# Optimization experiments

Measured on AMD Instinct MI355X. Metric: run time of the kernel, lower is better.

The kernel has to match this reference:

```python
import jax, jax.numpy as jnp
import numpy as np

D_MODEL = 1024
N_HEADS = 16
D_K = D_MODEL // N_HEADS


def setup_inputs() -> dict:
    key = jax.random.key(0)
    ks = jax.random.split(key, 9)
    s = 0.02
    x = jax.random.normal(ks[0], (2, 2048, D_MODEL), dtype=jnp.float32)
    Wq = jax.random.normal(ks[1], (D_MODEL, D_MODEL), dtype=jnp.float32) * s
    bq = jax.random.normal(ks[2], (D_MODEL,), dtype=jnp.float32) * s
    Wk = jax.random.normal(ks[3], (D_MODEL, D_MODEL), dtype=jnp.float32) * s
    bk = jax.random.normal(ks[4], (D_MODEL,), dtype=jnp.float32) * s
    Wv = jax.random.normal(ks[5], (D_MODEL, D_MODEL), dtype=jnp.float32) * s
    bv = jax.random.normal(ks[6], (D_MODEL,), dtype=jnp.float32) * s
    Wo = jax.random.normal(ks[7], (D_MODEL, D_MODEL), dtype=jnp.float32) * s
    bo = jax.random.normal(ks[8], (D_MODEL,), dtype=jnp.float32) * s
    return {"x": x, "Wq": Wq, "bq": bq, "Wk": Wk, "bk": bk,
            "Wv": Wv, "bv": bv, "Wo": Wo, "bo": bo}


def reference(x, Wq, bq, Wk, bk, Wv, bv, Wo, bo):
    B, S, D = x.shape
    # nn.Linear: y = x @ W.T + b
    q = x @ Wq.T + bq  # [B,S,D]
    k = x @ Wk.T + bk
    v = x @ Wv.T + bv
    # split heads -> [B,H,S,dk]
    q = q.reshape(B, S, N_HEADS, D_K).transpose(0, 2, 1, 3)
    k = k.reshape(B, S, N_HEADS, D_K).transpose(0, 2, 1, 3)
    v = v.reshape(B, S, N_HEADS, D_K).transpose(0, 2, 1, 3)
    scale = 1.0 / jnp.sqrt(jnp.asarray(D_K, dtype=x.dtype))
    scores = jnp.einsum('bhqd,bhkd->bhqk', q, k) * scale  # [B,H,S,S]
    weights = jax.nn.softmax(scores, axis=-1)
    out = jnp.einsum('bhqk,bhkd->bhqd', weights, v)  # [B,H,S,dk]
    concat = out.transpose(0, 2, 1, 3).reshape(B, S, D)
    return concat @ Wo.T + bo
```

## Files before the change

kernel.cpp:

```cpp
#include <hip/hip_runtime.h>

typedef unsigned short ushort_t;
typedef __attribute__((ext_vector_type(8))) __bf16 bf16x8;
typedef __attribute__((ext_vector_type(4))) short short4v;
typedef __attribute__((ext_vector_type(4))) float floatx4;

#define AS1 __attribute__((address_space(1)))
#define AS3 __attribute__((address_space(3)))

#define D_MODEL 1024
#define NH 16
#define DKH 64
#define SEQ 2048
#define NB 2
#define MTOT (NB * SEQ)

#define QSCALE 0.18033688011112042f

#define OFF_X   0u
#define OFF_WQ  4194304u
#define OFF_BQ  5242880u
#define OFF_WK  5243904u
#define OFF_BK  6292480u
#define OFF_WV  6293504u
#define OFF_BV  7342080u
#define OFF_WO  7343104u
#define OFF_BO  8391680u
#define CVT_TOT 8392704u

#define MFMA16(a, b, c) __builtin_amdgcn_mfma_f32_16x16x16bf16_1k((a), (b), (c), 0, 0, 0)

__device__ __forceinline__ float bf2f(ushort_t u) {
    union { unsigned u; float f; } v; v.u = ((unsigned)u) << 16; return v.f;
}
__device__ __forceinline__ ushort_t f2bf(float f) {
    union { float f; unsigned u; } v; v.f = f;
    unsigned r = v.u + 0x7FFFu + ((v.u >> 16) & 1u);
    return (ushort_t)(r >> 16);
}
__device__ __forceinline__ unsigned pack2bf(float a, float b) {
    unsigned ua = __float_as_uint(a), ub = __float_as_uint(b);
    ua = ua + 0x7FFFu + ((ua >> 16) & 1u);
    ub = ub + 0x7FFFu + ((ub >> 16) & 1u);
    return __builtin_amdgcn_perm(ub, ua, 0x07060302);
}
__device__ __forceinline__ short4v pack4bf(floatx4 v) {
    union { uint2 u; short4v s; } cv;
    cv.u.x = pack2bf(v[0], v[1]);
    cv.u.y = pack2bf(v[2], v[3]);
    return cv.s;
}

__global__ __launch_bounds__(256) void convert_kernel(
    const float* __restrict__ x,  const float* __restrict__ wq, const float* __restrict__ bq_,
    const float* __restrict__ wk, const float* __restrict__ bk_, const float* __restrict__ wv,
    const float* __restrict__ bv_, const float* __restrict__ wo, const float* __restrict__ bo_,
    ushort_t* __restrict__ dst)
{
    const unsigned idx = ((unsigned)blockIdx.x * 256u + threadIdx.x) * 4u;
    if (idx >= CVT_TOT) return;
    const float* src; unsigned off;
    if      (idx < OFF_WQ) { src = x;   off = idx - OFF_X;  }
    else if (idx < OFF_BQ) { src = wq;  off = idx - OFF_WQ; }
    else if (idx < OFF_WK) { src = bq_; off = idx - OFF_BQ; }
    else if (idx < OFF_BK) { src = wk;  off = idx - OFF_WK; }
    else if (idx < OFF_WV) { src = bk_; off = idx - OFF_BK; }
    else if (idx < OFF_BV) { src = wv;  off = idx - OFF_WV; }
    else if (idx < OFF_WO) { src = bv_; off = idx - OFF_BV; }
    else if (idx < OFF_BO) { src = wo;  off = idx - OFF_WO; }
    else                   { src = bo_; off = idx - OFF_BO; }
    float4 v = *reinterpret_cast<const float4*>(src + off);
    uint2 p;
    p.x = pack2bf(v.x, v.y);
    p.y = pack2bf(v.z, v.w);
    *reinterpret_cast<uint2*>(dst + idx) = p;
}

__device__ __forceinline__ void gemm_core(
    const ushort_t* __restrict__ X, const ushort_t* __restrict__ W,
    int m0, int n0, ushort_t* lds, floatx4 acc[4][4])
{
    const int tid = threadIdx.x;
    const int lane = tid & 63, wv = tid >> 6;
    const int wm = (wv >> 1) * 64, wn = (wv & 1) * 64;
    const int l15 = lane & 15, quad = lane >> 4;
    const floatx4 z4 = {0.f, 0.f, 0.f, 0.f};
#pragma unroll
    for (int i = 0; i < 4; ++i)
#pragma unroll
        for (int j = 0; j < 4; ++j) acc[i][j] = z4;
    const int lrow = lane >> 2;
    const int lcol = (lane & 3) * 8;
    const ushort_t* gA = X + (size_t)(m0 + lrow) * D_MODEL + lcol;
    const ushort_t* gB = W + (size_t)(n0 + lrow) * D_MODEL + lcol;
    for (int k0 = 0; k0 < D_MODEL; k0 += 64) {
        __syncthreads();
#pragma unroll
        for (int j = 0; j < 2; ++j) {
            const int r0 = (wv * 2 + j) * 16;
            __builtin_amdgcn_global_load_lds(
                (const AS1 unsigned*)(gA + (size_t)r0 * D_MODEL + k0),
                (AS3 unsigned*)(lds + r0 * 32), 16, 0, 0);
            __builtin_amdgcn_global_load_lds(
                (const AS1 unsigned*)(gA + (size_t)r0 * D_MODEL + k0 + 32),
                (AS3 unsigned*)(lds + 4096 + r0 * 32), 16, 0, 0);
            __builtin_amdgcn_global_load_lds(
                (const AS1 unsigned*)(gB + (size_t)r0 * D_MODEL + k0),
                (AS3 unsigned*)(lds + 8192 + r0 * 32), 16, 0, 0);
            __builtin_amdgcn_global_load_lds(
                (const AS1 unsigned*)(gB + (size_t)r0 * D_MODEL + k0 + 32),
                (AS3 unsigned*)(lds + 12288 + r0 * 32), 16, 0, 0);
        }
        asm volatile("s_waitcnt vmcnt(0)" ::: "memory");
        __syncthreads();
#pragma unroll
        for (int ks = 0; ks < 2; ++ks) {
            const ushort_t* A = lds + ks * 4096;
            const ushort_t* B = lds + 8192 + ks * 4096;
            bf16x8 af[4], bfr[4];
#pragma unroll
            for (int i = 0; i < 4; ++i)
                af[i] = *reinterpret_cast<const bf16x8*>(A + (wm + i * 16 + l15) * 32 + quad * 8);
#pragma unroll
            for (int j = 0; j < 4; ++j)
                bfr[j] = *reinterpret_cast<const bf16x8*>(B + (wn + j * 16 + l15) * 32 + quad * 8);
#pragma unroll
            for (int i = 0; i < 4; ++i)
#pragma unroll
                for (int j = 0; j < 4; ++j)
                    acc[i][j] = __builtin_amdgcn_mfma_f32_16x16x32_bf16(af[i], bfr[j], acc[i][j], 0, 0, 0);
        }
    }
}

__global__ __launch_bounds__(256, 3) void qkv_kernel(
    const ushort_t* __restrict__ x,
    const ushort_t* __restrict__ Wq, const ushort_t* __restrict__ bq,
    const ushort_t* __restrict__ Wk, const ushort_t* __restrict__ bk,
    const ushort_t* __restrict__ Wv, const ushort_t* __restrict__ bv,
    ushort_t* __restrict__ q_ws, ushort_t* __restrict__ k_ws, ushort_t* __restrict__ vt_ws)
{
    __shared__ __align__(16) ushort_t lds[17408];
    const int m0 = blockIdx.x * 128;
    const int which = blockIdx.y >> 3;
    const int n0 = (blockIdx.y & 7) * 128;
    const ushort_t* W    = (which == 0) ? Wq : (which == 1) ? Wk : Wv;
    const ushort_t* bias = (which == 0) ? bq : (which == 1) ? bk : bv;
    floatx4 acc[4][4];
    gemm_core(x, W, m0, n0, lds, acc);
    const int tid = threadIdx.x, lane = tid & 63, wv = tid >> 6;
    const int wm = (wv >> 1) * 64, wn = (wv & 1) * 64;
    const int l15 = lane & 15, quad = lane >> 4;
    const int b0 = m0 >> 11;
    const int s0 = m0 & (SEQ - 1);
    __syncthreads();
    if (which < 2) {
        ushort_t* Ts = lds;
        ushort_t* dst = (which == 0) ? q_ws : k_ws;
        const float scl = (which == 0) ? QSCALE : 1.0f;
#pragma unroll
        for (int j = 0; j < 4; ++j) {
            int coln = wn + j * 16 + l15;
            float bb = bf2f(bias[n0 + coln]);
#pragma unroll
            for (int i = 0; i < 4; ++i)
#pragma unroll
                for (int r = 0; r < 4; ++r) {
                    int rowm = wm + i * 16 + quad * 4 + r;
                    Ts[rowm * 136 + coln] = f2bf((acc[i][j][r] + bb) * scl);
                }
        }
        __syncthreads();
#pragma unroll
        for (int i = 0; i < 8; ++i) {
            int c = tid + 256 * i;
            int rowm = c >> 4, chunk = c & 15;
            float4 v = *reinterpret_cast<const float4*>(Ts + rowm * 136 + chunk * 8);
            int s = s0 + rowm;
            int n = n0 + chunk * 8, h = n >> 6, d = n & 63;
            *reinterpret_cast<float4*>(dst + (((size_t)(b0 * NH + h)) * SEQ + s) * DKH + d) = v;
        }
    } else {
        ushort_t* Ts = lds;
#pragma unroll
        for (int j = 0; j < 4; ++j) {
            int coln = wn + j * 16 + l15;
            float bb = bf2f(bias[n0 + coln]);
#pragma unroll
            for (int i = 0; i < 4; ++i)
#pragma unroll
                for (int r = 0; r < 4; ++r) {
                    int rowm = wm + i * 16 + quad * 4 + r;
                    Ts[coln * 136 + rowm] = f2bf(acc[i][j][r] + bb);
                }
        }
        __syncthreads();
#pragma unroll
        for (int i = 0; i < 8; ++i) {
            int c = tid + 256 * i;
            int nr = c >> 4, mc = (c & 15) * 8;
            float4 v = *reinterpret_cast<const float4*>(Ts + nr * 136 + mc);
            int n = n0 + nr, h = n >> 6, d = n & 63;
            *reinterpret_cast<float4*>(vt_ws + (((size_t)(b0 * NH + h)) * DKH + d) * SEQ + s0 + mc) = v;
        }
    }
}

__global__ __launch_bounds__(512, 4) void attn_kernel(
    const ushort_t* __restrict__ q_ws, const ushort_t* __restrict__ k_ws,
    const ushort_t* __restrict__ vt_ws, ushort_t* __restrict__ concat)
{
    __shared__ __align__(16) ushort_t sm[18432];
    const int qb = blockIdx.x, bh = blockIdx.y;
    const int tid = threadIdx.x;
    const int lane = tid & 63, wv = tid >> 6;
    const int half = wv >> 2, wq = wv & 3;
    const int l15 = lane & 15, quad = lane >> 4;
    const int ht = tid & 255;

    const ushort_t* Qg = q_ws + ((size_t)bh * SEQ + qb * 128) * DKH;
    const ushort_t* Kg = k_ws + ((size_t)bh * SEQ + half * (SEQ / 2)) * DKH;
    const ushort_t* Vg = vt_ws + (size_t)bh * DKH * SEQ + half * (SEQ / 2);

    ushort_t* Ks  = sm + half * 4608;
    ushort_t* VTs = sm + 9216 + half * 4608;

    const int r0c = ht >> 3,         c0c = (ht & 7) * 8;
    const int r1c = (ht + 256) >> 3, c1c = ((ht + 256) & 7) * 8;

    bf16x8 aq[2][2];
#pragma unroll
    for (int nt = 0; nt < 2; ++nt)
#pragma unroll
        for (int ks = 0; ks < 2; ++ks)
            aq[nt][ks] = *reinterpret_cast<const bf16x8*>(
                Qg + (size_t)(wq * 32 + nt * 16 + l15) * DKH + ks * 32 + quad * 8);

    const floatx4 z4 = {0.f, 0.f, 0.f, 0.f};
    floatx4 o[2][4];
    floatx4 la4[2] = {z4, z4};
#pragma unroll
    for (int nt = 0; nt < 2; ++nt)
#pragma unroll
        for (int dt = 0; dt < 4; ++dt) o[nt][dt] = z4;

    float4 pk0 = *reinterpret_cast<const float4*>(Kg + (size_t)r0c * DKH + c0c);
    float4 pk1 = *reinterpret_cast<const float4*>(Kg + (size_t)r1c * DKH + c1c);
    float4 pv0 = *reinterpret_cast<const float4*>(Vg + (size_t)r0c * SEQ + c0c);
    float4 pv1 = *reinterpret_cast<const float4*>(Vg + (size_t)r1c * SEQ + c1c);

    for (int t = 0; t < 16; ++t) {
        __syncthreads();
        *reinterpret_cast<float4*>(Ks + r0c * 72 + c0c) = pk0;
        *reinterpret_cast<float4*>(Ks + r1c * 72 + c1c) = pk1;
        *reinterpret_cast<float4*>(VTs + r0c * 72 + c0c) = pv0;
        *reinterpret_cast<float4*>(VTs + r1c * 72 + c1c) = pv1;
        __syncthreads();
        if (t < 15) {
            int toff = (t + 1) * 64;
            pk0 = *reinterpret_cast<const float4*>(Kg + (size_t)(toff + r0c) * DKH + c0c);
            pk1 = *reinterpret_cast<const float4*>(Kg + (size_t)(toff + r1c) * DKH + c1c);
            pv0 = *reinterpret_cast<const float4*>(Vg + (size_t)r0c * SEQ + toff + c0c);
            pv1 = *reinterpret_cast<const float4*>(Vg + (size_t)r1c * SEQ + toff + c1c);
        }

        floatx4 st[2][4];
#pragma unroll
        for (int nt = 0; nt < 2; ++nt)
#pragma unroll
            for (int mt = 0; mt < 4; ++mt) st[nt][mt] = z4;
#pragma unroll
        for (int ks = 0; ks < 2; ++ks)
#pragma unroll
            for (int mt = 0; mt < 4; ++mt) {
                bf16x8 akf = *reinterpret_cast<const bf16x8*>(Ks + (mt * 16 + l15) * 72 + ks * 32 + quad * 8);
                st[0][mt] = __builtin_amdgcn_mfma_f32_16x16x32_bf16(akf, aq[0][ks], st[0][mt], 0, 0, 0);
                st[1][mt] = __builtin_amdgcn_mfma_f32_16x16x32_bf16(akf, aq[1][ks], st[1][mt], 0, 0, 0);
            }

        short4v pb[2][4];
#pragma unroll
        for (int nt = 0; nt < 2; ++nt)
#pragma unroll
            for (int mt = 0; mt < 4; ++mt) {
#pragma unroll
                for (int r = 0; r < 4; ++r) st[nt][mt][r] = exp2f(st[nt][mt][r]);
                la4[nt] += st[nt][mt];
                pb[nt][mt] = pack4bf(st[nt][mt]);
            }

#pragma unroll
        for (int mt = 0; mt < 4; ++mt)
#pragma unroll
            for (int dt = 0; dt < 4; ++dt) {
                short4v av = *reinterpret_cast<const short4v*>(VTs + (dt * 16 + l15) * 72 + mt * 16 + quad * 4);
                o[0][dt] = MFMA16(av, pb[0][mt], o[0][dt]);
                o[1][dt] = MFMA16(av, pb[1][mt], o[1][dt]);
            }
    }
    float lsum[2];
#pragma unroll
    for (int nt = 0; nt < 2; ++nt) {
        float s = la4[nt][0] + la4[nt][1] + la4[nt][2] + la4[nt][3];
        s += __shfl_xor(s, 16, 64);
        s += __shfl_xor(s, 32, 64);
        lsum[nt] = s;
    }
    __syncthreads();
    float* Of = (float*)sm;
    float* lf = Of + 64 * 130;
    if (half == 1) {
#pragma unroll
        for (int nt = 0; nt < 2; ++nt) {
            int q = wq * 32 + nt * 16 + l15;
            if (quad == 0) lf[q] = lsum[nt];
#pragma unroll
            for (int dt = 0; dt < 4; ++dt)
#pragma unroll
                for (int r = 0; r < 4; ++r)
                    Of[(dt * 16 + quad * 4 + r) * 130 + q] = o[nt][dt][r];
        }
    }
    __syncthreads();
    if (half == 0) {
        const int b0 = bh >> 4, h = bh & 15;
#pragma unroll
        for (int nt = 0; nt < 2; ++nt) {
            int q = wq * 32 + nt * 16 + l15;
            float linv = 1.f / (lsum[nt] + lf[q]);
            size_t base = ((size_t)(b0 * SEQ + qb * 128 + q)) * D_MODEL + h * DKH;
#pragma unroll
            for (int dt = 0; dt < 4; ++dt) {
                float f0 = (o[nt][dt][0] + Of[(dt * 16 + quad * 4 + 0) * 130 + q]) * linv;
                float f1 = (o[nt][dt][1] + Of[(dt * 16 + quad * 4 + 1) * 130 + q]) * linv;
                float f2 = (o[nt][dt][2] + Of[(dt * 16 + quad * 4 + 2) * 130 + q]) * linv;
                float f3 = (o[nt][dt][3] + Of[(dt * 16 + quad * 4 + 3) * 130 + q]) * linv;
                uint2 pk;
                pk.x = pack2bf(f0, f1);
                pk.y = pack2bf(f2, f3);
                *reinterpret_cast<uint2*>(concat + base + dt * 16 + quad * 4) = pk;
            }
        }
    }
}

__global__ __launch_bounds__(256, 3) void oproj_kernel(
    const ushort_t* __restrict__ cc, const ushort_t* __restrict__ Wo,
    const ushort_t* __restrict__ bo, float* __restrict__ out)
{
    __shared__ __align__(16) ushort_t lds[4 * 128 * 32];
    const int m0 = blockIdx.x * 128, n0 = blockIdx.y * 128;
    floatx4 acc[4][4];
    gemm_core(cc, Wo, m0, n0, lds, acc);
    const int tid = threadIdx.x, lane = tid & 63, wv = tid >> 6;
    const int wm = (wv >> 1) * 64, wn = (wv & 1) * 64;
    const int l15 = lane & 15, quad = lane >> 4;
#pragma unroll
    for (int j = 0; j < 4; ++j) {
        int n = n0 + wn + j * 16 + l15;
        float bb = bf2f(bo[n]);
#pragma unroll
        for (int i = 0; i < 4; ++i)
#pragma unroll
            for (int r = 0; r < 4; ++r) {
                int m = m0 + wm + i * 16 + quad * 4 + r;
                out[(size_t)m * D_MODEL + n] = acc[i][j][r] + bb;
            }
    }
}

extern "C" void kernel_launch(void* const* d_in, const int* in_sizes, int n_in,
                              void* d_out, int out_size, void* d_ws, size_t ws_size,
                              hipStream_t stream)
{
    ushort_t* cvt = (ushort_t*)d_ws;
    const ushort_t* xb  = cvt + OFF_X;
    const ushort_t* Wqb = cvt + OFF_WQ;
    const ushort_t* bqb = cvt + OFF_BQ;
    const ushort_t* Wkb = cvt + OFF_WK;
    const ushort_t* bkb = cvt + OFF_BK;
    const ushort_t* Wvb = cvt + OFF_WV;
    const ushort_t* bvb = cvt + OFF_BV;
    const ushort_t* Wob = cvt + OFF_WO;
    const ushort_t* bob = cvt + OFF_BO;
    ushort_t* q_ws   = cvt + CVT_TOT;
    ushort_t* k_ws   = q_ws  + (size_t)MTOT * D_MODEL;
    ushort_t* vt_ws  = k_ws  + (size_t)MTOT * D_MODEL;
    ushort_t* concat = vt_ws + (size_t)MTOT * D_MODEL;

    convert_kernel<<<(CVT_TOT / 1024), 256, 0, stream>>>(
        (const float*)d_in[0], (const float*)d_in[1], (const float*)d_in[2],
        (const float*)d_in[3], (const float*)d_in[4], (const float*)d_in[5],
        (const float*)d_in[6], (const float*)d_in[7], (const float*)d_in[8], cvt);
    qkv_kernel<<<dim3(32, 24), 256, 0, stream>>>(xb, Wqb, bqb, Wkb, bkb, Wvb, bvb, q_ws, k_ws, vt_ws);
    attn_kernel<<<dim3(16, 32), 512, 0, stream>>>(q_ws, k_ws, vt_ws, concat);
    oproj_kernel<<<dim3(32, 8), 256, 0, stream>>>(concat, Wob, bob, (float*)d_out);
}
```

Before: 210.4 us.

## Route attention probabilities through LDS to use 16x16x32 MFMA for PV

The PV product previously fed exp'd scores straight from registers into 16x16x16 MFMAs, using the transposed layout that the score MFMA produced. Each wave now writes its bf16 probability tile to a private LDS region and reads it back in K-major bf16x8 fragments. That lets PV run on the wider 16x16x32 MFMA with halved instruction count, and Q is now staged through LDS as well. The trade-off is doubled shared memory (72KB per block), which may cut occupancy below the launch-bounds target, plus extra LDS traffic per tile. The epilogue layout also changes, with per-element scalar bf16 stores to concat instead of packed stores.

After: 210.0 us. Within noise of the previous version (-0.2%).

```diff
diff --git a/kernel.cpp b/kernel.cpp
--- a/kernel.cpp
+++ b/kernel.cpp
@@ -2,7 +2,6 @@
 
 typedef unsigned short ushort_t;
 typedef __attribute__((ext_vector_type(8))) __bf16 bf16x8;
-typedef __attribute__((ext_vector_type(4))) short short4v;
 typedef __attribute__((ext_vector_type(4))) float floatx4;
 
 #define AS1 __attribute__((address_space(1)))
@@ -28,8 +27,6 @@
 #define OFF_BO  8391680u
 #define CVT_TOT 8392704u
 
-#define MFMA16(a, b, c) __builtin_amdgcn_mfma_f32_16x16x16bf16_1k((a), (b), (c), 0, 0, 0)
-
 __device__ __forceinline__ float bf2f(ushort_t u) {
     union { unsigned u; float f; } v; v.u = ((unsigned)u) << 16; return v.f;
 }
@@ -43,12 +40,6 @@
     ua = ua + 0x7FFFu + ((ua >> 16) & 1u);
     ub = ub + 0x7FFFu + ((ub >> 16) & 1u);
     return __builtin_amdgcn_perm(ub, ua, 0x07060302);
-}
-__device__ __forceinline__ short4v pack4bf(floatx4 v) {
-    union { uint2 u; short4v s; } cv;
-    cv.u.x = pack2bf(v[0], v[1]);
-    cv.u.y = pack2bf(v[2], v[3]);
-    return cv.s;
 }
 
 __global__ __launch_bounds__(256) void convert_kernel(
@@ -210,7 +201,7 @@
     const ushort_t* __restrict__ q_ws, const ushort_t* __restrict__ k_ws,
     const ushort_t* __restrict__ vt_ws, ushort_t* __restrict__ concat)
 {
-    __shared__ __align__(16) ushort_t sm[18432];
+    __shared__ __align__(16) ushort_t sm[36864];
     const int qb = blockIdx.x, bh = blockIdx.y;
     const int tid = threadIdx.x;
     const int lane = tid & 63, wv = tid >> 6;
@@ -222,19 +213,28 @@
     const ushort_t* Kg = k_ws + ((size_t)bh * SEQ + half * (SEQ / 2)) * DKH;
     const ushort_t* Vg = vt_ws + (size_t)bh * DKH * SEQ + half * (SEQ / 2);
 
-    ushort_t* Ks  = sm + half * 4608;
-    ushort_t* VTs = sm + 9216 + half * 4608;
+    ushort_t* Ks     = sm + half * 4608;
+    ushort_t* VTs    = sm + 9216 + half * 4608;
+    ushort_t* Ps     = sm + 18432 + wv * 2304;
+    ushort_t* Qstage = sm + 18432;
 
     const int r0c = ht >> 3,         c0c = (ht & 7) * 8;
     const int r1c = (ht + 256) >> 3, c1c = ((ht + 256) & 7) * 8;
 
+#pragma unroll
+    for (int i = 0; i < 2; ++i) {
+        int c = tid + 512 * i;
+        int row = c >> 3, col = (c & 7) * 8;
+        *reinterpret_cast<float4*>(Qstage + row * 72 + col) =
+            *reinterpret_cast<const float4*>(Qg + row * DKH + col);
+    }
+    __syncthreads();
     bf16x8 aq[2][2];
 #pragma unroll
     for (int nt = 0; nt < 2; ++nt)
 #pragma unroll
         for (int ks = 0; ks < 2; ++ks)
-            aq[nt][ks] = *reinterpret_cast<const bf16x8*>(
-                Qg + (size_t)(wq * 32 + nt * 16 + l15) * DKH + ks * 32 + quad * 8);
+            aq[nt][ks] = *reinterpret_cast<const bf16x8*>(Qstage + (wq * 32 + nt * 16 + l15) * 72 + ks * 32 + quad * 8);
 
     const floatx4 z4 = {0.f, 0.f, 0.f, 0.f};
     floatx4 o[2][4];
@@ -278,7 +278,6 @@
                 st[1][mt] = __builtin_amdgcn_mfma_f32_16x16x32_bf16(akf, aq[1][ks], st[1][mt], 0, 0, 0);
             }
 
-        short4v pb[2][4];
 #pragma unroll
         for (int nt = 0; nt < 2; ++nt)
 #pragma unroll
@@ -286,17 +285,23 @@
 #pragma unroll
                 for (int r = 0; r < 4; ++r) st[nt][mt][r] = exp2f(st[nt][mt][r]);
                 la4[nt] += st[nt][mt];
-                pb[nt][mt] = pack4bf(st[nt][mt]);
-            }
-
-#pragma unroll
-        for (int mt = 0; mt < 4; ++mt)
+                uint2 pk;
+                pk.x = pack2bf(st[nt][mt][0], st[nt][mt][1]);
+                pk.y = pack2bf(st[nt][mt][2], st[nt][mt][3]);
+                *reinterpret_cast<uint2*>(Ps + (nt * 16 + l15) * 72 + mt * 16 + quad * 4) = pk;
+            }
+        asm volatile("s_waitcnt lgkmcnt(0)" ::: "memory");
+#pragma unroll
+        for (int ks = 0; ks < 2; ++ks) {
+            bf16x8 ap0 = *reinterpret_cast<const bf16x8*>(Ps + l15 * 72 + ks * 32 + quad * 8);
+            bf16x8 ap1 = *reinterpret_cast<const bf16x8*>(Ps + (16 + l15) * 72 + ks * 32 + quad * 8);
 #pragma unroll
             for (int dt = 0; dt < 4; ++dt) {
-                short4v av = *reinterpret_cast<const short4v*>(VTs + (dt * 16 + l15) * 72 + mt * 16 + quad * 4);
-                o[0][dt] = MFMA16(av, pb[0][mt], o[0][dt]);
-                o[1][dt] = MFMA16(av, pb[1][mt], o[1][dt]);
-            }
+                bf16x8 bvv = *reinterpret_cast<const bf16x8*>(VTs + (dt * 16 + l15) * 72 + ks * 32 + quad * 8);
+                o[0][dt] = __builtin_amdgcn_mfma_f32_16x16x32_bf16(ap0, bvv, o[0][dt], 0, 0, 0);
+                o[1][dt] = __builtin_amdgcn_mfma_f32_16x16x32_bf16(ap1, bvv, o[1][dt], 0, 0, 0);
+            }
+        }
     }
     float lsum[2];
 #pragma unroll
@@ -308,17 +313,18 @@
     }
     __syncthreads();
     float* Of = (float*)sm;
-    float* lf = Of + 64 * 130;
+    float* lf = Of + 128 * 68;
     if (half == 1) {
 #pragma unroll
         for (int nt = 0; nt < 2; ++nt) {
-            int q = wq * 32 + nt * 16 + l15;
-            if (quad == 0) lf[q] = lsum[nt];
-#pragma unroll
-            for (int dt = 0; dt < 4; ++dt)
-#pragma unroll
-                for (int r = 0; r < 4; ++r)
-                    Of[(dt * 16 + quad * 4 + r) * 130 + q] = o[nt][dt][r];
+            if (quad == 0) lf[wq * 32 + nt * 16 + l15] = lsum[nt];
+#pragma unroll
+            for (int r = 0; r < 4; ++r) {
+                int row = wq * 32 + nt * 16 + quad * 4 + r;
+#pragma unroll
+                for (int dt = 0; dt < 4; ++dt)
+                    Of[row * 68 + dt * 16 + l15] = o[nt][dt][r];
+            }
         }
     }
     __syncthreads();
@@ -326,19 +332,18 @@
         const int b0 = bh >> 4, h = bh & 15;
 #pragma unroll
         for (int nt = 0; nt < 2; ++nt) {
-            int q = wq * 32 + nt * 16 + l15;
-            float linv = 1.f / (lsum[nt] + lf[q]);
-            size_t base = ((size_t)(b0 * SEQ + qb * 128 + q)) * D_MODEL + h * DKH;
-#pragma unroll
-            for (int dt = 0; dt < 4; ++dt) {
-                float f0 = (o[nt][dt][0] + Of[(dt * 16 + quad * 4 + 0) * 130 + q]) * linv;
-                float f1 = (o[nt][dt][1] + Of[(dt * 16 + quad * 4 + 1) * 130 + q]) * linv;
-                float f2 = (o[nt][dt][2] + Of[(dt * 16 + quad * 4 + 2) * 130 + q]) * linv;
-                float f3 = (o[nt][dt][3] + Of[(dt * 16 + quad * 4 + 3) * 130 + q]) * linv;
-                uint2 pk;
-                pk.x = pack2bf(f0, f1);
-                pk.y = pack2bf(f2, f3);
-                *reinterpret_cast<uint2*>(concat + base + dt * 16 + quad * 4) = pk;
+            float ltot = lsum[nt] + lf[wq * 32 + nt * 16 + l15];
+            float linv = 1.f / ltot;
+#pragma unroll
+            for (int r = 0; r < 4; ++r) {
+                float lB = __shfl(linv, quad * 4 + r, 64);
+                int row = wq * 32 + nt * 16 + quad * 4 + r;
+                size_t base = ((size_t)(b0 * SEQ + qb * 128 + row)) * D_MODEL + h * DKH;
+#pragma unroll
+                for (int dt = 0; dt < 4; ++dt) {
+                    float sum = o[nt][dt][r] + Of[row * 68 + dt * 16 + l15];
+                    concat[base + dt * 16 + l15] = f2bf(sum * lB);
+                }
             }
         }
     }
```
